# Performance work log

Measured on AMD Instinct MI355X. Metric: run time of the kernel, lower is better.

The kernel has to match this reference:

```python
import jax, jax.numpy as jnp
import numpy as np

B, C, D = 32768, 4, 64   # batch, in_channels, input_size
T, O = 16, 32            # num_tokens, output_size


def setup_inputs() -> dict:
    key = jax.random.key(0)
    kx, kw, kb, km = jax.random.split(key, 4)
    # torch Linear default init ~ U(-1/sqrt(fan_in), 1/sqrt(fan_in)); use scaled normals
    x = jax.random.normal(kx, (B, C, D), dtype=jnp.float32)
    W_gen = jax.random.normal(kw, (T, O, D), dtype=jnp.float32) / np.sqrt(D)
    b_gen = jax.random.normal(kb, (T, O), dtype=jnp.float32) / np.sqrt(D)      # their biases
    W_merge = jax.random.normal(km, (T, C), dtype=jnp.float32) / np.sqrt(C)
    return {"x": x, "W_gen": W_gen, "b_gen": b_gen, "W_merge": W_merge}


def reference(x, W_gen, b_gen, W_merge):
    # For each token i: t = x @ W_gen[i].T + b_gen[i]  -> [B, C, O]
    #                   merge over channels: relu(t.permute(0,2,1) @ W_merge[i]) -> [B, O]
    # Batched over all 16 tokens with einsum (one grouped GEMM each).
    t = jnp.einsum('bcd,tod->btco', x, W_gen) + b_gen[None, :, None, :]  # [B, T, C, O]
    tokens = jax.nn.relu(jnp.einsum('btco,tc->bto', t, W_merge))          # [B, T, O]
    return tokens.reshape(B, T, -1)
```

## Files before the change

### kernel.cpp

```cpp
#include <hip/hip_runtime.h>
#include <hip/hip_bf16.h>

typedef __attribute__((ext_vector_type(8))) short  short8;
typedef __attribute__((ext_vector_type(4))) float  floatx4;

#define MFMA16(a, b, c) __builtin_amdgcn_mfma_f32_16x16x32_bf16((a), (b), (c), 0, 0, 0)

__device__ __forceinline__ short f2bf(float f) {
    unsigned u = __builtin_bit_cast(unsigned, f);
    u += 0x7fffu + ((u >> 16) & 1u);
    return (short)(u >> 16);
}

constexpr int kB       = 32768;
constexpr int kC       = 4;
constexpr int kD       = 64;
constexpr int kT       = 16;
constexpr int kO       = 32;
constexpr int kNCol    = kT * kO;
constexpr int kRows    = 16;
constexpr int kGrid    = 1024;
constexpr int kTiles   = (kB / kRows) / kGrid;

__global__ __launch_bounds__(256) void tok_kernel(
    const float* __restrict__ x,
    const float* __restrict__ Wg,
    const float* __restrict__ bg,
    const float* __restrict__ Wm,
    float* __restrict__ out)
{
    const int tid  = threadIdx.x;
    const int lane = tid & 63;
    const int wv   = tid >> 6;
    const int l15  = lane & 15;
    const int lg   = lane >> 4;
    const int t0   = wv * 4;

    short8 bfrag[4][2][2];
    float  wmv[4][4];
    float  biasv[4][2];
#pragma unroll
    for (int tt = 0; tt < 4; ++tt) {
        const int t = t0 + tt;
        float S = 0.f;
#pragma unroll
        for (int c = 0; c < kC; ++c) { wmv[tt][c] = Wm[t*kC + c]; S += wmv[tt][c]; }
#pragma unroll
        for (int nf = 0; nf < 2; ++nf) {
            biasv[tt][nf] = bg[t*kO + nf*16 + l15] * S;
#pragma unroll
            for (int ks = 0; ks < 2; ++ks) {
                const float* src = Wg + (size_t)(t*kO + nf*16 + l15)*kD + ks*32 + lg*8;
                floatx4 a = *reinterpret_cast<const floatx4*>(src);
                floatx4 b = *reinterpret_cast<const floatx4*>(src + 4);
                short8 f;
                f[0]=f2bf(a[0]); f[1]=f2bf(a[1]); f[2]=f2bf(a[2]); f[3]=f2bf(a[3]);
                f[4]=f2bf(b[0]); f[5]=f2bf(b[1]); f[6]=f2bf(b[2]); f[7]=f2bf(b[3]);
                bfrag[tt][nf][ks] = f;
            }
        }
    }

#pragma unroll 1
    for (int it = 0; it < kTiles; ++it) {
        const int tile = blockIdx.x + it*kGrid;
        const int brow = tile*kRows + l15;
        const float* xr = x + (size_t)brow * (kC*kD);

        float xv[2][kC][8];
#pragma unroll
        for (int ks = 0; ks < 2; ++ks)
#pragma unroll
        for (int c = 0; c < kC; ++c) {
            const float* p = xr + c*kD + ks*32 + lg*8;
            floatx4 lo = *reinterpret_cast<const floatx4*>(p);
            floatx4 hi = *reinterpret_cast<const floatx4*>(p + 4);
            xv[ks][c][0]=lo[0]; xv[ks][c][1]=lo[1]; xv[ks][c][2]=lo[2]; xv[ks][c][3]=lo[3];
            xv[ks][c][4]=hi[0]; xv[ks][c][5]=hi[1]; xv[ks][c][6]=hi[2]; xv[ks][c][7]=hi[3];
        }

        floatx4 acc0[4] = {{0.f,0.f,0.f,0.f},{0.f,0.f,0.f,0.f},{0.f,0.f,0.f,0.f},{0.f,0.f,0.f,0.f}};
        floatx4 acc1[4] = {{0.f,0.f,0.f,0.f},{0.f,0.f,0.f,0.f},{0.f,0.f,0.f,0.f},{0.f,0.f,0.f,0.f}};

#pragma unroll
        for (int tt = 0; tt < 4; ++tt) {
#pragma unroll
            for (int ks = 0; ks < 2; ++ks) {
                short8 af;
#pragma unroll
                for (int j = 0; j < 8; ++j) {
                    float v = xv[ks][0][j] * wmv[tt][0];
                    v = fmaf(xv[ks][1][j], wmv[tt][1], v);
                    v = fmaf(xv[ks][2][j], wmv[tt][2], v);
                    v = fmaf(xv[ks][3][j], wmv[tt][3], v);
                    af[j] = f2bf(v);
                }
                acc0[tt] = MFMA16(af, bfrag[tt][0][ks], acc0[tt]);
                acc1[tt] = MFMA16(af, bfrag[tt][1][ks], acc1[tt]);
            }
        }

        const int bbase = tile*kRows + lg*4;
#pragma unroll
        for (int tt = 0; tt < 4; ++tt) {
            const int t = t0 + tt;
#pragma unroll
            for (int nf = 0; nf < 2; ++nf) {
                const int col = t*kO + nf*16 + l15;
                const float bia = biasv[tt][nf];
#pragma unroll
                for (int r = 0; r < 4; ++r) {
                    float v = (nf == 0 ? acc0[tt][r] : acc1[tt][r]) + bia;
                    v = v > 0.f ? v : 0.f;
                    out[(size_t)(bbase + r)*kNCol + col] = v;
                }
            }
        }
    }
}

extern "C" void kernel_launch(void* const* d_in, const int* in_sizes, int n_in,
                              void* d_out, int out_size, void* d_ws, size_t ws_size,
                              hipStream_t stream)
{
    const float* x  = (const float*)d_in[0];
    const float* Wg = (const float*)d_in[1];
    const float* bg = (const float*)d_in[2];
    const float* Wm = (const float*)d_in[3];
    float* out = (float*)d_out;
    tok_kernel<<<kGrid, 256, 0, stream>>>(x, Wg, bg, Wm, out);
}
```

Before: 126.8 us.

## Stage x tile through padded LDS with coalesced loads, one tile per block

Each block now handles a single 16-row tile, and the grid is doubled to 2048 so the persistent loop is gone. The x tile is loaded with fully coalesced 16-byte-per-lane global reads into a padded shared-memory buffer, then read back in MFMA fragment layout. The x loads are issued before the weight-fragment setup so that global latency overlaps the weight conversion. The cost is that every block repeats the weight load and bf16 conversion, plus an extra LDS round-trip and a barrier.

```diff
diff --git a/kernel.cpp b/kernel.cpp
--- a/kernel.cpp
+++ b/kernel.cpp
@@ -12,23 +12,24 @@
     return (short)(u >> 16);
 }
 
-constexpr int kB       = 32768;
-constexpr int kC       = 4;
-constexpr int kD       = 64;
-constexpr int kT       = 16;
-constexpr int kO       = 32;
-constexpr int kNCol    = kT * kO;
-constexpr int kRows    = 16;
-constexpr int kGrid    = 1024;
-constexpr int kTiles   = (kB / kRows) / kGrid;
+constexpr int kC     = 4;
+constexpr int kD     = 64;
+constexpr int kT     = 16;
+constexpr int kO     = 32;
+constexpr int kNCol  = kT * kO;
+constexpr int kPad   = 260;
+constexpr int kGrid  = 2048;
+constexpr int kThr   = 256;
 
-__global__ __launch_bounds__(256) void tok_kernel(
+__global__ __launch_bounds__(kThr) void tok_kernel(
     const float* __restrict__ x,
     const float* __restrict__ Wg,
     const float* __restrict__ bg,
     const float* __restrict__ Wm,
     float* __restrict__ out)
 {
+    __shared__ alignas(16) float lds[16][kPad];
+
     const int tid  = threadIdx.x;
     const int lane = tid & 63;
     const int wv   = tid >> 6;
@@ -36,84 +37,95 @@
     const int lg   = lane >> 4;
     const int t0   = wv * 4;
 
+    const int tile = blockIdx.x;
+
+    floatx4 stg[4];
+#pragma unroll
+    for (int i = 0; i < 4; ++i) {
+        const int grow = tile * 16 + i * 4 + wv;
+        stg[i] = *reinterpret_cast<const floatx4*>(
+            (const char*)x + (size_t)grow * 1024 + (unsigned)lane * 16);
+    }
+
+    float  wmv[4][4];
     short8 bfrag[4][2][2];
-    float  wmv[4][4];
     float  biasv[4][2];
 #pragma unroll
     for (int tt = 0; tt < 4; ++tt) {
         const int t = t0 + tt;
-        float S = 0.f;
+        float s = 0.f;
 #pragma unroll
-        for (int c = 0; c < kC; ++c) { wmv[tt][c] = Wm[t*kC + c]; S += wmv[tt][c]; }
+        for (int c = 0; c < kC; ++c) { wmv[tt][c] = Wm[t * kC + c]; s += wmv[tt][c]; }
 #pragma unroll
         for (int nf = 0; nf < 2; ++nf) {
-            biasv[tt][nf] = bg[t*kO + nf*16 + l15] * S;
+            biasv[tt][nf] = bg[t * kO + nf * 16 + l15] * s;
 #pragma unroll
             for (int ks = 0; ks < 2; ++ks) {
-                const float* src = Wg + (size_t)(t*kO + nf*16 + l15)*kD + ks*32 + lg*8;
+                const float* src = Wg + (size_t)(t * kO + nf * 16 + l15) * kD + ks * 32 + lg * 8;
                 floatx4 a = *reinterpret_cast<const floatx4*>(src);
                 floatx4 b = *reinterpret_cast<const floatx4*>(src + 4);
                 short8 f;
-                f[0]=f2bf(a[0]); f[1]=f2bf(a[1]); f[2]=f2bf(a[2]); f[3]=f2bf(a[3]);
-                f[4]=f2bf(b[0]); f[5]=f2bf(b[1]); f[6]=f2bf(b[2]); f[7]=f2bf(b[3]);
+                f[0] = f2bf(a[0]); f[1] = f2bf(a[1]); f[2] = f2bf(a[2]); f[3] = f2bf(a[3]);
+                f[4] = f2bf(b[0]); f[5] = f2bf(b[1]); f[6] = f2bf(b[2]); f[7] = f2bf(b[3]);
                 bfrag[tt][nf][ks] = f;
             }
         }
     }
 
-#pragma unroll 1
-    for (int it = 0; it < kTiles; ++it) {
-        const int tile = blockIdx.x + it*kGrid;
-        const int brow = tile*kRows + l15;
-        const float* xr = x + (size_t)brow * (kC*kD);
+#pragma unroll
+    for (int i = 0; i < 4; ++i) {
+        const int row = i * 4 + wv;
+        *reinterpret_cast<floatx4*>(
+            (char*)&lds[row][0] + (unsigned)lane * 16) = stg[i];
+    }
+    __syncthreads();
 
-        float xv[2][kC][8];
+    floatx4 acc[4][2] = {};
+    const char* rowp = (const char*)&lds[l15][0];
 #pragma unroll
-        for (int ks = 0; ks < 2; ++ks)
+    for (int ks = 0; ks < 2; ++ks) {
+        floatx4 xlo[4], xhi[4];
 #pragma unroll
-        for (int c = 0; c < kC; ++c) {
-            const float* p = xr + c*kD + ks*32 + lg*8;
-            floatx4 lo = *reinterpret_cast<const floatx4*>(p);
-            floatx4 hi = *reinterpret_cast<const floatx4*>(p + 4);
-            xv[ks][c][0]=lo[0]; xv[ks][c][1]=lo[1]; xv[ks][c][2]=lo[2]; xv[ks][c][3]=lo[3];
-            xv[ks][c][4]=hi[0]; xv[ks][c][5]=hi[1]; xv[ks][c][6]=hi[2]; xv[ks][c][7]=hi[3];
+        for (int c = 0; c < 4; ++c) {
+            const unsigned q = (unsigned)(c * 256 + ks * 128 + lg * 32);
+            xlo[c] = *reinterpret_cast<const floatx4*>(rowp + q);
+            xhi[c] = *reinterpret_cast<const floatx4*>(rowp + q + 16u);
         }
-
-        floatx4 acc0[4] = {{0.f,0.f,0.f,0.f},{0.f,0.f,0.f,0.f},{0.f,0.f,0.f,0.f},{0.f,0.f,0.f,0.f}};
-        floatx4 acc1[4] = {{0.f,0.f,0.f,0.f},{0.f,0.f,0.f,0.f},{0.f,0.f,0.f,0.f},{0.f,0.f,0.f,0.f}};
-
 #pragma unroll
         for (int tt = 0; tt < 4; ++tt) {
+            short8 af;
 #pragma unroll
-            for (int ks = 0; ks < 2; ++ks) {
-                short8 af;
+            for (int j = 0; j < 4; ++j) {
+                float v = xlo[0][j] * wmv[tt][0];
+                v = fmaf(xlo[1][j], wmv[tt][1], v);
+                v = fmaf(xlo[2][j], wmv[tt][2], v);
+                v = fmaf(xlo[3][j], wmv[tt][3], v);
+                af[j] = f2bf(v);
+            }
 #pragma unroll
-                for (int j = 0; j < 8; ++j) {
-                    float v = xv[ks][0][j] * wmv[tt][0];
-                    v = fmaf(xv[ks][1][j], wmv[tt][1], v);
-                    v = fmaf(xv[ks][2][j], wmv[tt][2], v);
-                    v = fmaf(xv[ks][3][j], wmv[tt][3], v);
-                    af[j] = f2bf(v);
-                }
-                acc0[tt] = MFMA16(af, bfrag[tt][0][ks], acc0[tt]);
-                acc1[tt] = MFMA16(af, bfrag[tt][1][ks], acc1[tt]);
+            for (int j = 0; j < 4; ++j) {
+                float v = xhi[0][j] * wmv[tt][0];
+                v = fmaf(xhi[1][j], wmv[tt][1], v);
+                v = fmaf(xhi[2][j], wmv[tt][2], v);
+                v = fmaf(xhi[3][j], wmv[tt][3], v);
+                af[4 + j] = f2bf(v);
             }
+            acc[tt][0] = MFMA16(af, bfrag[tt][0][ks], acc[tt][0]);
+            acc[tt][1] = MFMA16(af, bfrag[tt][1][ks], acc[tt][1]);
         }
+    }
 
-        const int bbase = tile*kRows + lg*4;
+    const int rowbase = tile * 16 + lg * 4;
 #pragma unroll
-        for (int tt = 0; tt < 4; ++tt) {
-            const int t = t0 + tt;
+    for (int tt = 0; tt < 4; ++tt) {
 #pragma unroll
-            for (int nf = 0; nf < 2; ++nf) {
-                const int col = t*kO + nf*16 + l15;
-                const float bia = biasv[tt][nf];
+        for (int nf = 0; nf < 2; ++nf) {
+            const int col = (t0 + tt) * kO + nf * 16 + l15;
+            const float bia = biasv[tt][nf];
 #pragma unroll
-                for (int r = 0; r < 4; ++r) {
-                    float v = (nf == 0 ? acc0[tt][r] : acc1[tt][r]) + bia;
-                    v = v > 0.f ? v : 0.f;
-                    out[(size_t)(bbase + r)*kNCol + col] = v;
-                }
+            for (int r = 0; r < 4; ++r) {
+                float v = acc[tt][nf][r] + bia;
+                out[(size_t)(rowbase + r) * kNCol + col] = v > 0.f ? v : 0.f;
             }
         }
     }
@@ -128,5 +140,5 @@
     const float* bg = (const float*)d_in[2];
     const float* Wm = (const float*)d_in[3];
     float* out = (float*)d_out;
-    tok_kernel<<<kGrid, 256, 0, stream>>>(x, Wg, bg, Wm, out);
+    tok_kernel<<<kGrid, kThr, 0, stream>>>(x, Wg, bg, Wm, out);
 }
```

Result: faster. 120.1 us (-5.3%).
